# Kernel optimization log

Hardware: AMD Instinct MI355X
Metric: run time of the kernel (lower is better)

Reference implementation:

```python
import math
import jax, jax.numpy as jnp
import numpy as np

HEAD_SIZE = 64
DEPTH = 0

def lambda_init_fn(depth):
    depth = depth + 1
    return 0.8 - 0.6 * math.exp(-0.3 * depth)

def setup_inputs() -> dict:
    key = jax.random.key(0)
    ks = jax.random.split(key, 9)
    B, T, C = 4, 4096, 1024
    H2 = 2 * HEAD_SIZE  # 128
    return {
        "x":  jax.random.normal(ks[0], (B, T, C), dtype=jnp.float32),
        "Wq": jax.random.normal(ks[1], (C, H2), dtype=jnp.float32) * (C ** -0.5),
        "Wk": jax.random.normal(ks[2], (C, H2), dtype=jnp.float32) * (C ** -0.5),
        "Wv": jax.random.normal(ks[3], (C, H2), dtype=jnp.float32) * (C ** -0.5),
        "lambda_q1": jax.random.normal(ks[4], (HEAD_SIZE,), dtype=jnp.float32) * 0.1,
        "lambda_q2": jax.random.normal(ks[5], (HEAD_SIZE,), dtype=jnp.float32) * 0.1,
        "lambda_k1": jax.random.normal(ks[6], (HEAD_SIZE,), dtype=jnp.float32) * 0.1,
        "lambda_k2": jax.random.normal(ks[7], (HEAD_SIZE,), dtype=jnp.float32) * 0.1,
    }

def reference(x, Wq, Wk, Wv, lambda_q1, lambda_q2, lambda_k1, lambda_k2):
    B, T, C = x.shape
    q = x @ Wq  # (B,T,2*hs)
    k = x @ Wk
    v = x @ Wv  # (B,T,2*hs)
    q1, q2 = jnp.split(q, 2, axis=-1)
    k1, k2 = jnp.split(k, 2, axis=-1)
    scale = 1.0 / math.sqrt(HEAD_SIZE)
    w1 = jnp.einsum('btd,bsd->bts', q1, k1) * scale  # (B,T,T)
    w2 = jnp.einsum('btd,bsd->bts', q2, k2) * scale
    causal = jnp.tril(jnp.ones((T, T), dtype=bool))
    neg_inf = jnp.float32(-jnp.inf)
    w1 = jnp.where(causal, w1, neg_inf)
    w2 = jnp.where(causal, w2, neg_inf)
    lam1 = jnp.exp(jnp.sum(lambda_q1 * lambda_k1))
    lam2 = jnp.exp(jnp.sum(lambda_q2 * lambda_k2))
    lam = lam1 - lam2 + lambda_init_fn(DEPTH)
    weights = jax.nn.softmax(w1, axis=-1) - lam * jax.nn.softmax(w2, axis=-1)
    out = jnp.einsum('bts,bsd->btd', weights, v)  # (B,T,2*hs)
    return out
```

## Files before the change

### kernel.cpp

```cpp
#include <hip/hip_runtime.h>
#include <hip/hip_bf16.h>

typedef __bf16 bf16x8 __attribute__((ext_vector_type(8)));
typedef float f32x4 __attribute__((ext_vector_type(4)));

#define LAMBDA_INIT 0.3555090675909693f
#define CEXP 0.18033688011112042f

#define K_OFF   ((size_t)16384 * 128)
#define VT_OFF  ((size_t)2 * 16384 * 128)
#define PART_OFF_BYTES ((size_t)12582912)
#define REC_FLOATS 4160

__device__ __forceinline__ unsigned short f2bf(float f) {
    __hip_bfloat16 h = __float2bfloat16(f);
    unsigned short u;
    __builtin_memcpy(&u, &h, 2);
    return u;
}
__device__ __forceinline__ float bf2f(unsigned short u) {
    unsigned int x = ((unsigned int)u) << 16;
    float f;
    __builtin_memcpy(&f, &x, 4);
    return f;
}
__device__ __forceinline__ unsigned int cvt_pk_bf16(float a, float b) {
    unsigned int r;
    asm volatile("v_cvt_pk_bf16_f32 %0, %1, %2" : "=v"(r) : "v"(a), "v"(b));
    return r;
}

__global__ __launch_bounds__(256) void prep_wt(
    const float* __restrict__ Wq, const float* __restrict__ Wk,
    const float* __restrict__ Wv, unsigned short* __restrict__ WT) {
    const int kt = blockIdx.x, nt = blockIdx.y, mat = blockIdx.z;
    const float* W = (mat == 0) ? Wq : (mat == 1) ? Wk : Wv;
    unsigned short* O = WT + (size_t)mat * 128 * 1024;
    __shared__ float tb[64][65];
    const int r = threadIdx.x >> 2, c4 = (threadIdx.x & 3) * 16;
    for (int j = 0; j < 4; ++j) {
        float4 v = *(const float4*)&W[(size_t)(kt * 64 + r) * 128 + nt * 64 + c4 + j * 4];
        tb[r][c4 + j * 4 + 0] = v.x;
        tb[r][c4 + j * 4 + 1] = v.y;
        tb[r][c4 + j * 4 + 2] = v.z;
        tb[r][c4 + j * 4 + 3] = v.w;
    }
    __syncthreads();
    unsigned short tmp[16];
    for (int j = 0; j < 16; ++j) tmp[j] = f2bf(tb[c4 + j][r]);
    *(uint4*)&O[(size_t)(nt * 64 + r) * 1024 + kt * 64 + c4] = *(uint4*)&tmp[0];
    *(uint4*)&O[(size_t)(nt * 64 + r) * 1024 + kt * 64 + c4 + 8] = *(uint4*)&tmp[8];
}

__global__ __launch_bounds__(256) void qkv_gemm(
    const float* __restrict__ x, const unsigned short* __restrict__ WT,
    unsigned short* __restrict__ qkv) {
    const int tid = threadIdx.x;
    const int l = tid & 63, w = tid >> 6;
    const int g = l >> 4, i16 = l & 15;
    const int row0 = blockIdx.x * 64;
    const int mat = blockIdx.y;
    const unsigned short* Wt = WT + (size_t)mat * 128 * 1024;

    __shared__ unsigned short xs[64][72];
    __shared__ unsigned short wt[128][72];

    f32x4 acc[8];
    const f32x4 z4 = {0.f, 0.f, 0.f, 0.f};
    for (int nb = 0; nb < 8; ++nb) acc[nb] = z4;

    const int xr = tid >> 4;
    const int xc = (tid & 15) * 4;
    const int wn = tid >> 3;
    const int wk8 = (tid & 7) * 8;
    const float* xp0 = &x[(size_t)(row0 + xr) * 1024 + xc];
    const unsigned short* wp0 = &Wt[(size_t)wn * 1024 + wk8];

    float4 fx0, fx1, fx2, fx3;
    uint4 fw0, fw1, fw2, fw3;

#define QKV_ISSUE(k0_) do {                                                 \
        fx0 = *(const float4*)&xp0[(k0_)];                                  \
        fx1 = *(const float4*)&xp0[16 * 1024 + (k0_)];                      \
        fx2 = *(const float4*)&xp0[32 * 1024 + (k0_)];                      \
        fx3 = *(const float4*)&xp0[48 * 1024 + (k0_)];                      \
        fw0 = *(const uint4*)&wp0[(k0_)];                                   \
        fw1 = *(const uint4*)&wp0[32 * 1024 + (k0_)];                       \
        fw2 = *(const uint4*)&wp0[64 * 1024 + (k0_)];                       \
        fw3 = *(const uint4*)&wp0[96 * 1024 + (k0_)];                       \
    } while (0)

#define QKV_STORE() do {                                                    \
        *(ushort4*)&xs[xr +  0][xc] = make_ushort4(f2bf(fx0.x), f2bf(fx0.y), f2bf(fx0.z), f2bf(fx0.w)); \
        *(ushort4*)&xs[xr + 16][xc] = make_ushort4(f2bf(fx1.x), f2bf(fx1.y), f2bf(fx1.z), f2bf(fx1.w)); \
        *(ushort4*)&xs[xr + 32][xc] = make_ushort4(f2bf(fx2.x), f2bf(fx2.y), f2bf(fx2.z), f2bf(fx2.w)); \
        *(ushort4*)&xs[xr + 48][xc] = make_ushort4(f2bf(fx3.x), f2bf(fx3.y), f2bf(fx3.z), f2bf(fx3.w)); \
        *(uint4*)&wt[wn +  0][wk8] = fw0;                                   \
        *(uint4*)&wt[wn + 32][wk8] = fw1;                                   \
        *(uint4*)&wt[wn + 64][wk8] = fw2;                                   \
        *(uint4*)&wt[wn + 96][wk8] = fw3;                                   \
    } while (0)

    QKV_ISSUE(0);
    #pragma unroll 1
    for (int k0 = 0; k0 < 1024; k0 += 64) {
        __syncthreads();
        QKV_STORE();
        if (k0 + 64 < 1024) QKV_ISSUE(k0 + 64);
        __syncthreads();

        bf16x8 af0 = *(const bf16x8*)&xs[w * 16 + i16][8 * g];
        bf16x8 af1 = *(const bf16x8*)&xs[w * 16 + i16][32 + 8 * g];
        #pragma unroll
        for (int nb = 0; nb < 8; ++nb) {
            bf16x8 b0 = *(const bf16x8*)&wt[nb * 16 + i16][8 * g];
            bf16x8 b1 = *(const bf16x8*)&wt[nb * 16 + i16][32 + 8 * g];
            acc[nb] = __builtin_amdgcn_mfma_f32_16x16x32_bf16(af0, b0, acc[nb], 0, 0, 0);
            acc[nb] = __builtin_amdgcn_mfma_f32_16x16x32_bf16(af1, b1, acc[nb], 0, 0, 0);
        }
    }
#undef QKV_ISSUE
#undef QKV_STORE

    __syncthreads();
    unsigned short(*ts)[136] = (unsigned short(*)[136]) & wt[0][0];
    const float qscale = (mat == 0) ? CEXP : 1.0f;
    for (int nb = 0; nb < 8; ++nb)
        for (int r = 0; r < 4; ++r)
            ts[w * 16 + g * 4 + r][nb * 16 + i16] = f2bf(acc[nb][r] * qscale);
    __syncthreads();

    const int bq = row0 >> 12;
    const int s = (row0 >> 6) & 63;
    if (mat == 0) {
        unsigned short* outp = qkv + (size_t)row0 * 128;
        #pragma unroll
        for (int it = 0; it < 4; ++it) {
            int tr = it * 16 + (tid >> 4), dv0 = (tid & 15) * 8;
            *(uint4*)&outp[tr * 128 + dv0] = *(const uint4*)&ts[tr][dv0];
        }
    } else if (mat == 1) {
        unsigned short* kimg = qkv + K_OFF + ((size_t)(bq * 64 + s) * 2) * 4096;
        #pragma unroll
        for (int it = 0; it < 4; ++it) {
            int lin = it * 256 + tid;
            int branch_ = (lin >> 9) & 1;
            int region = (lin >> 6) & 7;
            int slot = lin & 63;
            int row = (region >> 1) * 16 + (slot & 15);
            int d = branch_ * 64 + (region & 1) * 32 + (slot >> 4) * 8;
            uint4 vv = *(const uint4*)&ts[row][d];
            *(uint4*)&kimg[(size_t)branch_ * 4096 + (region * 64 + slot) * 8] = vv;
        }
    } else {
        unsigned short* vimg = qkv + VT_OFF + (size_t)(bq * 64 + s) * 8192;
        #pragma unroll
        for (int it = 0; it < 4; ++it) {
            int lin = it * 256 + tid;
            int region = lin >> 6;
            int slot = lin & 63;
            int dv = (region >> 1) * 16 + (slot & 15);
            int kv0 = (region & 1) * 32 + (slot >> 4) * 8;
            unsigned short tmp[8];
            #pragma unroll
            for (int e = 0; e < 8; ++e) tmp[e] = ts[kv0 + e][dv];
            *(uint4*)&vimg[(region * 64 + slot) * 8] = *(uint4*)tmp;
        }
    }
}

__global__ __launch_bounds__(256, 3) void diff_attn_pair(
    const unsigned short* __restrict__ q, const unsigned short* __restrict__ kimg,
    const unsigned short* __restrict__ vimg,
    float* __restrict__ part, int ncs) {
    const int bx = blockIdx.x, b = blockIdx.y;
    const int c = blockIdx.z >> 1, branch = blockIdx.z & 1;
    const int bxe = (c & 1) ? (31 - bx) : bx;
    const int t_o = 63 - 2 * bxe, t_e = t_o - 1;
    const int n = t_o + 1;
    const int s_lo = (c * n) >> ncs, smax = ((c + 1) * n) >> ncs;

    if (s_lo >= smax) return;

    const int tid = threadIdx.x;
    const int l = tid & 63, w = tid >> 6;
    const int gq = l >> 4, i16 = l & 15;
    const float NEGINF = -__builtin_inff();

    __shared__ unsigned short ksf[4096];
    __shared__ unsigned short psf[8192];

    float* recA = part + ((((size_t)(b * 64 + t_e) << ncs) + c) * 2 + branch) * REC_FLOATS;
    float* recB = part + ((((size_t)(b * 64 + t_o) << ncs) + c) * 2 + branch) * REC_FLOATS;
    const bool emptyA = (s_lo > t_e);

    const size_t bbase = (size_t)b * 4096;
    const unsigned short* kimg_b = kimg + (size_t)b * 524288;
    const unsigned short* vimg_b = vimg + (size_t)b * 524288;
    const int tid8 = tid * 8;
    const int l8 = l * 8;
    const f32x4 z4 = {0.f, 0.f, 0.f, 0.f};

    bf16x8 qfA[2], qfB[2];
    #pragma unroll
    for (int cc = 0; cc < 2; ++cc) {
        qfA[cc] = *(const bf16x8*)&q[(bbase + t_e * 64 + w * 16 + i16) * 128 + branch * 64 + cc * 32 + 8 * gq];
        qfB[cc] = *(const bf16x8*)&q[(bbase + t_o * 64 + w * 16 + i16) * 128 + branch * 64 + cc * 32 + 8 * gq];
    }

    float lsumA = 0.f, lsumB = 0.f;
    f32x4 acc[2][4][2];
    for (int qs = 0; qs < 2; ++qs)
        for (int qg = 0; qg < 4; ++qg)
            for (int j = 0; j < 2; ++j) acc[qs][qg][j] = z4;

    int pdst[4];
    #pragma unroll
    for (int cb = 0; cb < 4; ++cb)
        pdst[cb] = ((w * 2 + (cb >> 1)) * 64 + ((cb & 1) * 2 + (gq >> 1)) * 16 + i16) * 8 + (gq & 1) * 4;

    uint4 kr0, kr1;
    bf16x8 vb00, vb01, vb10, vb11;

#define K_ISSUE(s_) do {                                                            \
        const unsigned short* kp = &kimg_b[((size_t)(s_) * 2 + branch) * 4096];     \
        kr0 = *(const uint4*)&kp[tid8];                                             \
        kr1 = *(const uint4*)&kp[tid8 + 2048];                                      \
    } while (0)
#define V_ISSUE(s_) do {                                                            \
        const unsigned short* vp = &vimg_b[(size_t)(s_) * 8192 + w * 2048];         \
        vb00 = *(const bf16x8*)&vp[l8];                                             \
        vb01 = *(const bf16x8*)&vp[512 + l8];                                       \
        vb10 = *(const bf16x8*)&vp[1024 + l8];                                      \
        vb11 = *(const bf16x8*)&vp[1536 + l8];                                      \
    } while (0)

    K_ISSUE(s_lo);
    V_ISSUE(s_lo);
    #pragma unroll 1
    for (int s = s_lo; s < smax; ++s) {
        __syncthreads();
        *(uint4*)&ksf[tid8] = kr0;
        *(uint4*)&ksf[tid8 + 2048] = kr1;
        if (s + 1 < smax) K_ISSUE(s + 1);
        __syncthreads();
        const bool aAct = (s != t_o);

        if (aAct) {
            f32x4 sc[4];
            for (int cb = 0; cb < 4; ++cb) sc[cb] = z4;
            __builtin_amdgcn_s_setprio(1);
            #pragma unroll
            for (int cb = 0; cb < 4; ++cb)
                for (int cc = 0; cc < 2; ++cc) {
                    bf16x8 kf = *(const bf16x8*)&ksf[((cb * 2 + cc) * 64 + l) * 8];
                    sc[cb] = __builtin_amdgcn_mfma_f32_16x16x32_bf16(kf, qfA[cc], sc[cb], 0, 0, 0);
                }
            __builtin_amdgcn_s_setprio(0);
            if (s == t_e) {
                int ql = w * 16 + i16;
                for (int cb = 0; cb < 4; ++cb)
                    for (int r = 0; r < 4; ++r)
                        if (cb * 16 + gq * 4 + r > ql) sc[cb][r] = NEGINF;
            }
            #pragma unroll
            for (int cb = 0; cb < 4; ++cb) {
                float p0 = exp2f(sc[cb][0]);
                float p1 = exp2f(sc[cb][1]);
                float p2 = exp2f(sc[cb][2]);
                float p3 = exp2f(sc[cb][3]);
                lsumA += (p0 + p1) + (p2 + p3);
                uint2 pw;
                pw.x = cvt_pk_bf16(p0, p1);
                pw.y = cvt_pk_bf16(p2, p3);
                *(uint2*)&psf[pdst[cb]] = pw;
            }
        }
        {
            f32x4 sc[4];
            for (int cb = 0; cb < 4; ++cb) sc[cb] = z4;
            __builtin_amdgcn_s_setprio(1);
            #pragma unroll
            for (int cb = 0; cb < 4; ++cb)
                for (int cc = 0; cc < 2; ++cc) {
                    bf16x8 kf = *(const bf16x8*)&ksf[((cb * 2 + cc) * 64 + l) * 8];
                    sc[cb] = __builtin_amdgcn_mfma_f32_16x16x32_bf16(kf, qfB[cc], sc[cb], 0, 0, 0);
                }
            __builtin_amdgcn_s_setprio(0);
            if (s == t_o) {
                int ql = w * 16 + i16;
                for (int cb = 0; cb < 4; ++cb)
                    for (int r = 0; r < 4; ++r)
                        if (cb * 16 + gq * 4 + r > ql) sc[cb][r] = NEGINF;
            }
            #pragma unroll
            for (int cb = 0; cb < 4; ++cb) {
                float p0 = exp2f(sc[cb][0]);
                float p1 = exp2f(sc[cb][1]);
                float p2 = exp2f(sc[cb][2]);
                float p3 = exp2f(sc[cb][3]);
                lsumB += (p0 + p1) + (p2 + p3);
                uint2 pw;
                pw.x = cvt_pk_bf16(p0, p1);
                pw.y = cvt_pk_bf16(p2, p3);
                *(uint2*)&psf[4096 + pdst[cb]] = pw;
            }
        }
        __syncthreads();

        __builtin_amdgcn_s_setprio(1);
        if (aAct) {
            #pragma unroll
            for (int qg = 0; qg < 4; ++qg) {
                bf16x8 pa0 = *(const bf16x8*)&psf[(qg * 2 + 0) * 512 + l8];
                bf16x8 pa1 = *(const bf16x8*)&psf[(qg * 2 + 1) * 512 + l8];
                acc[0][qg][0] = __builtin_amdgcn_mfma_f32_16x16x32_bf16(pa0, vb00, acc[0][qg][0], 0, 0, 0);
                acc[0][qg][0] = __builtin_amdgcn_mfma_f32_16x16x32_bf16(pa1, vb01, acc[0][qg][0], 0, 0, 0);
                acc[0][qg][1] = __builtin_amdgcn_mfma_f32_16x16x32_bf16(pa0, vb10, acc[0][qg][1], 0, 0, 0);
                acc[0][qg][1] = __builtin_amdgcn_mfma_f32_16x16x32_bf16(pa1, vb11, acc[0][qg][1], 0, 0, 0);
            }
        }
        #pragma unroll
        for (int qg = 0; qg < 4; ++qg) {
            bf16x8 pa0 = *(const bf16x8*)&psf[4096 + (qg * 2 + 0) * 512 + l8];
            bf16x8 pa1 = *(const bf16x8*)&psf[4096 + (qg * 2 + 1) * 512 + l8];
            acc[1][qg][0] = __builtin_amdgcn_mfma_f32_16x16x32_bf16(pa0, vb00, acc[1][qg][0], 0, 0, 0);
            acc[1][qg][0] = __builtin_amdgcn_mfma_f32_16x16x32_bf16(pa1, vb01, acc[1][qg][0], 0, 0, 0);
            acc[1][qg][1] = __builtin_amdgcn_mfma_f32_16x16x32_bf16(pa0, vb10, acc[1][qg][1], 0, 0, 0);
            acc[1][qg][1] = __builtin_amdgcn_mfma_f32_16x16x32_bf16(pa1, vb11, acc[1][qg][1], 0, 0, 0);
        }
        __builtin_amdgcn_s_setprio(0);
        if (s + 1 < smax) V_ISSUE(s + 1);
    }
#undef K_ISSUE
#undef V_ISSUE

    lsumA += __shfl_xor(lsumA, 16);
    lsumA += __shfl_xor(lsumA, 32);
    lsumB += __shfl_xor(lsumB, 16);
    lsumB += __shfl_xor(lsumB, 32);
    if (!emptyA) {
        if (gq == 0) recA[w * 16 + i16] = lsumA;
        unsigned short* OA = (unsigned short*)(recA + 64);
        for (int qg = 0; qg < 4; ++qg)
            for (int j = 0; j < 2; ++j)
                for (int r = 0; r < 4; ++r)
                    OA[(qg * 16 + gq * 4 + r) * 128 + (w * 2 + j) * 16 + i16] = f2bf(acc[0][qg][j][r]);
    }
    {
        if (gq == 0) recB[w * 16 + i16] = lsumB;
        unsigned short* OB = (unsigned short*)(recB + 64);
        for (int qg = 0; qg < 4; ++qg)
            for (int j = 0; j < 2; ++j)
                for (int r = 0; r < 4; ++r)
                    OB[(qg * 16 + gq * 4 + r) * 128 + (w * 2 + j) * 16 + i16] = f2bf(acc[1][qg][j][r]);
    }
}

__global__ __launch_bounds__(256) void diff_combine(
    const float* __restrict__ part,
    const float* __restrict__ lq1, const float* __restrict__ lq2,
    const float* __restrict__ lk1, const float* __restrict__ lk2,
    float* __restrict__ out, int ncs) {
    const int t = blockIdx.x, b = blockIdx.y;
    const int tid = threadIdx.x;
    const int nc = 1 << ncs;
    const int n = (t | 1) + 1;
    __shared__ float sl[2][64];
    __shared__ float s_lam;

    const float* recbase = part + (((size_t)(b * 64 + t) << ncs)) * 2 * REC_FLOATS;

    if (tid < 64) {
        float s1 = lq1[tid] * lk1[tid];
        float s2 = lq2[tid] * lk2[tid];
        for (int off = 32; off > 0; off >>= 1) {
            s1 += __shfl_xor(s1, off);
            s2 += __shfl_xor(s2, off);
        }
        if (tid == 0) s_lam = expf(s1) - expf(s2) + LAMBDA_INIT;
    }
    if (tid < 128) {
        int r = tid & 63, br = tid >> 6;
        float acc = 0.f;
        for (int c = 0; c < nc; ++c) {
            int lo = (c * n) >> ncs, hi = ((c + 1) * n) >> ncs;
            if (lo >= hi || lo > t) continue;
            acc += recbase[(c * 2 + br) * REC_FLOATS + r];
        }
        sl[br][r] = acc;
    }
    __syncthreads();
    const float lam = s_lam;

    float* op = out + ((size_t)b * 4096 + (size_t)t * 64) * 128;
    for (int grp = 0; grp < 4; ++grp) {
        int gid = grp * 256 + tid;
        int e = gid * 8;
        int row = e >> 7;
        float o1[8] = {0, 0, 0, 0, 0, 0, 0, 0}, o2[8] = {0, 0, 0, 0, 0, 0, 0, 0};
        for (int c = 0; c < nc; ++c) {
            int lo = (c * n) >> ncs, hi = ((c + 1) * n) >> ncs;
            if (lo >= hi || lo > t) continue;
            const unsigned short* O0 = (const unsigned short*)(recbase + (c * 2 + 0) * REC_FLOATS + 64);
            const unsigned short* O1 = (const unsigned short*)(recbase + (c * 2 + 1) * REC_FLOATS + 64);
            uint4 u0 = *(const uint4*)&O0[e];
            uint4 u1 = *(const uint4*)&O1[e];
            const unsigned short* e0 = (const unsigned short*)&u0;
            const unsigned short* e1 = (const unsigned short*)&u1;
            #pragma unroll
            for (int j = 0; j < 8; ++j) {
                o1[j] += bf2f(e0[j]);
                o2[j] += bf2f(e1[j]);
            }
        }
        float l1inv = 1.0f / sl[0][row], l2inv = 1.0f / sl[1][row];
        float res[8];
        #pragma unroll
        for (int j = 0; j < 8; ++j) res[j] = o1[j] * l1inv - lam * o2[j] * l2inv;
        *(float4*)&op[e] = *(float4*)&res[0];
        *(float4*)&op[e + 4] = *(float4*)&res[4];
    }
}

extern "C" void kernel_launch(void* const* d_in, const int* in_sizes, int n_in,
                              void* d_out, int out_size, void* d_ws, size_t ws_size,
                              hipStream_t stream) {
    const float* x   = (const float*)d_in[0];
    const float* Wq  = (const float*)d_in[1];
    const float* Wk  = (const float*)d_in[2];
    const float* Wv  = (const float*)d_in[3];
    const float* lq1 = (const float*)d_in[4];
    const float* lq2 = (const float*)d_in[5];
    const float* lk1 = (const float*)d_in[6];
    const float* lk2 = (const float*)d_in[7];
    float* out = (float*)d_out;
    unsigned short* qkv = (unsigned short*)d_ws;

    const int ncs = 2;
    const size_t part_bytes = (size_t)256 * (1 << ncs) * 2 * REC_FLOATS * 4;
    float* part = (float*)((char*)d_ws + PART_OFF_BYTES);
    unsigned short* WT = (unsigned short*)((char*)d_ws + PART_OFF_BYTES + part_bytes);

    prep_wt<<<dim3(16, 2, 3), 256, 0, stream>>>(Wq, Wk, Wv, WT);
    qkv_gemm<<<dim3(256, 3), 256, 0, stream>>>(x, WT, qkv);

    const unsigned short* qb = qkv;
    const unsigned short* kb = qkv + K_OFF;
    const unsigned short* vtb = qkv + VT_OFF;
    diff_attn_pair<<<dim3(32, 4, 2 << ncs), 256, 0, stream>>>(qb, kb, vtb, part, ncs);
    diff_combine<<<dim3(64, 4), 256, 0, stream>>>(part, lq1, lq2, lk1, lk2, out, ncs);
}
```

Measured before the change: 96.18 us.

## Double-buffer K tile in attention and deepen QKV GEMM prefetch

The QKV projection GEMM now keeps two k-slabs of global loads in flight, using alternating register sets, and gets a 3-blocks-per-CU launch bound. In the attention kernel the K shared tile is double-buffered, which removes one barrier per step. The QK^T MFMAs for both query tiles are interleaved so they can share each K fragment load. In exchange the kernels use more registers and LDS, which could cut occupancy, and the A-tile QK MFMAs now run even on steps where that tile is inactive.

```diff
diff --git a/kernel.cpp b/kernel.cpp
--- a/kernel.cpp
+++ b/kernel.cpp
@@ -52,7 +52,7 @@
     *(uint4*)&O[(size_t)(nt * 64 + r) * 1024 + kt * 64 + c4 + 8] = *(uint4*)&tmp[8];
 }
 
-__global__ __launch_bounds__(256) void qkv_gemm(
+__global__ __launch_bounds__(256, 3) void qkv_gemm(
     const float* __restrict__ x, const unsigned short* __restrict__ WT,
     unsigned short* __restrict__ qkv) {
     const int tid = threadIdx.x;
@@ -76,51 +76,61 @@
     const float* xp0 = &x[(size_t)(row0 + xr) * 1024 + xc];
     const unsigned short* wp0 = &Wt[(size_t)wn * 1024 + wk8];
 
-    float4 fx0, fx1, fx2, fx3;
-    uint4 fw0, fw1, fw2, fw3;
-
-#define QKV_ISSUE(k0_) do {                                                 \
-        fx0 = *(const float4*)&xp0[(k0_)];                                  \
-        fx1 = *(const float4*)&xp0[16 * 1024 + (k0_)];                      \
-        fx2 = *(const float4*)&xp0[32 * 1024 + (k0_)];                      \
-        fx3 = *(const float4*)&xp0[48 * 1024 + (k0_)];                      \
-        fw0 = *(const uint4*)&wp0[(k0_)];                                   \
-        fw1 = *(const uint4*)&wp0[32 * 1024 + (k0_)];                       \
-        fw2 = *(const uint4*)&wp0[64 * 1024 + (k0_)];                       \
-        fw3 = *(const uint4*)&wp0[96 * 1024 + (k0_)];                       \
+    float4 ax0, ax1, ax2, ax3, bx0, bx1, bx2, bx3;
+    uint4 aw0, aw1, aw2, aw3, bw0, bw1, bw2, bw3;
+
+#define QI(k0_, X0, X1, X2, X3, W0, W1, W2, W3) do {                        \
+        X0 = *(const float4*)&xp0[(k0_)];                                   \
+        X1 = *(const float4*)&xp0[16 * 1024 + (k0_)];                       \
+        X2 = *(const float4*)&xp0[32 * 1024 + (k0_)];                       \
+        X3 = *(const float4*)&xp0[48 * 1024 + (k0_)];                       \
+        W0 = *(const uint4*)&wp0[(k0_)];                                    \
+        W1 = *(const uint4*)&wp0[32 * 1024 + (k0_)];                        \
+        W2 = *(const uint4*)&wp0[64 * 1024 + (k0_)];                        \
+        W3 = *(const uint4*)&wp0[96 * 1024 + (k0_)];                        \
     } while (0)
 
-#define QKV_STORE() do {                                                    \
-        *(ushort4*)&xs[xr +  0][xc] = make_ushort4(f2bf(fx0.x), f2bf(fx0.y), f2bf(fx0.z), f2bf(fx0.w)); \
-        *(ushort4*)&xs[xr + 16][xc] = make_ushort4(f2bf(fx1.x), f2bf(fx1.y), f2bf(fx1.z), f2bf(fx1.w)); \
-        *(ushort4*)&xs[xr + 32][xc] = make_ushort4(f2bf(fx2.x), f2bf(fx2.y), f2bf(fx2.z), f2bf(fx2.w)); \
-        *(ushort4*)&xs[xr + 48][xc] = make_ushort4(f2bf(fx3.x), f2bf(fx3.y), f2bf(fx3.z), f2bf(fx3.w)); \
-        *(uint4*)&wt[wn +  0][wk8] = fw0;                                   \
-        *(uint4*)&wt[wn + 32][wk8] = fw1;                                   \
-        *(uint4*)&wt[wn + 64][wk8] = fw2;                                   \
-        *(uint4*)&wt[wn + 96][wk8] = fw3;                                   \
+#define QS(X0, X1, X2, X3, W0, W1, W2, W3) do {                             \
+        *(ushort4*)&xs[xr +  0][xc] = make_ushort4(f2bf(X0.x), f2bf(X0.y), f2bf(X0.z), f2bf(X0.w)); \
+        *(ushort4*)&xs[xr + 16][xc] = make_ushort4(f2bf(X1.x), f2bf(X1.y), f2bf(X1.z), f2bf(X1.w)); \
+        *(ushort4*)&xs[xr + 32][xc] = make_ushort4(f2bf(X2.x), f2bf(X2.y), f2bf(X2.z), f2bf(X2.w)); \
+        *(ushort4*)&xs[xr + 48][xc] = make_ushort4(f2bf(X3.x), f2bf(X3.y), f2bf(X3.z), f2bf(X3.w)); \
+        *(uint4*)&wt[wn +  0][wk8] = W0;                                    \
+        *(uint4*)&wt[wn + 32][wk8] = W1;                                    \
+        *(uint4*)&wt[wn + 64][wk8] = W2;                                    \
+        *(uint4*)&wt[wn + 96][wk8] = W3;                                    \
     } while (0)
 
-    QKV_ISSUE(0);
+#define QMFMA() do {                                                        \
+        bf16x8 af0 = *(const bf16x8*)&xs[w * 16 + i16][8 * g];              \
+        bf16x8 af1 = *(const bf16x8*)&xs[w * 16 + i16][32 + 8 * g];         \
+        _Pragma("unroll")                                                   \
+        for (int nb = 0; nb < 8; ++nb) {                                    \
+            bf16x8 b0 = *(const bf16x8*)&wt[nb * 16 + i16][8 * g];          \
+            bf16x8 b1 = *(const bf16x8*)&wt[nb * 16 + i16][32 + 8 * g];     \
+            acc[nb] = __builtin_amdgcn_mfma_f32_16x16x32_bf16(af0, b0, acc[nb], 0, 0, 0); \
+            acc[nb] = __builtin_amdgcn_mfma_f32_16x16x32_bf16(af1, b1, acc[nb], 0, 0, 0); \
+        }                                                                   \
+    } while (0)
+
+    QI(0, ax0, ax1, ax2, ax3, aw0, aw1, aw2, aw3);
+    QI(64, bx0, bx1, bx2, bx3, bw0, bw1, bw2, bw3);
     #pragma unroll 1
-    for (int k0 = 0; k0 < 1024; k0 += 64) {
-        __syncthreads();
-        QKV_STORE();
-        if (k0 + 64 < 1024) QKV_ISSUE(k0 + 64);
-        __syncthreads();
-
-        bf16x8 af0 = *(const bf16x8*)&xs[w * 16 + i16][8 * g];
-        bf16x8 af1 = *(const bf16x8*)&xs[w * 16 + i16][32 + 8 * g];
-        #pragma unroll
-        for (int nb = 0; nb < 8; ++nb) {
-            bf16x8 b0 = *(const bf16x8*)&wt[nb * 16 + i16][8 * g];
-            bf16x8 b1 = *(const bf16x8*)&wt[nb * 16 + i16][32 + 8 * g];
-            acc[nb] = __builtin_amdgcn_mfma_f32_16x16x32_bf16(af0, b0, acc[nb], 0, 0, 0);
-            acc[nb] = __builtin_amdgcn_mfma_f32_16x16x32_bf16(af1, b1, acc[nb], 0, 0, 0);
-        }
-    }
-#undef QKV_ISSUE
-#undef QKV_STORE
+    for (int k0 = 0; k0 < 1024; k0 += 128) {
+        __syncthreads();
+        QS(ax0, ax1, ax2, ax3, aw0, aw1, aw2, aw3);
+        if (k0 + 128 < 1024) QI(k0 + 128, ax0, ax1, ax2, ax3, aw0, aw1, aw2, aw3);
+        __syncthreads();
+        QMFMA();
+        __syncthreads();
+        QS(bx0, bx1, bx2, bx3, bw0, bw1, bw2, bw3);
+        if (k0 + 192 < 1024) QI(k0 + 192, bx0, bx1, bx2, bx3, bw0, bw1, bw2, bw3);
+        __syncthreads();
+        QMFMA();
+    }
+#undef QI
+#undef QS
+#undef QMFMA
 
     __syncthreads();
     unsigned short(*ts)[136] = (unsigned short(*)[136]) & wt[0][0];
@@ -187,7 +197,7 @@
     const int gq = l >> 4, i16 = l & 15;
     const float NEGINF = -__builtin_inff();
 
-    __shared__ unsigned short ksf[4096];
+    __shared__ unsigned short ksf[2][4096];
     __shared__ unsigned short psf[8192];
 
     float* recA = part + ((((size_t)(b * 64 + t_e) << ncs) + c) * 2 + branch) * REC_FLOATS;
@@ -237,38 +247,40 @@
 
     K_ISSUE(s_lo);
     V_ISSUE(s_lo);
+    int pb = 0;
     #pragma unroll 1
     for (int s = s_lo; s < smax; ++s) {
-        __syncthreads();
-        *(uint4*)&ksf[tid8] = kr0;
-        *(uint4*)&ksf[tid8 + 2048] = kr1;
+        *(uint4*)&ksf[pb][tid8] = kr0;
+        *(uint4*)&ksf[pb][tid8 + 2048] = kr1;
         if (s + 1 < smax) K_ISSUE(s + 1);
         __syncthreads();
         const bool aAct = (s != t_o);
 
+        f32x4 scA[4], scB[4];
+        for (int cb = 0; cb < 4; ++cb) { scA[cb] = z4; scB[cb] = z4; }
+        __builtin_amdgcn_s_setprio(1);
+        #pragma unroll
+        for (int cb = 0; cb < 4; ++cb)
+            for (int cc = 0; cc < 2; ++cc) {
+                bf16x8 kf = *(const bf16x8*)&ksf[pb][((cb * 2 + cc) * 64 + l) * 8];
+                scA[cb] = __builtin_amdgcn_mfma_f32_16x16x32_bf16(kf, qfA[cc], scA[cb], 0, 0, 0);
+                scB[cb] = __builtin_amdgcn_mfma_f32_16x16x32_bf16(kf, qfB[cc], scB[cb], 0, 0, 0);
+            }
+        __builtin_amdgcn_s_setprio(0);
+
         if (aAct) {
-            f32x4 sc[4];
-            for (int cb = 0; cb < 4; ++cb) sc[cb] = z4;
-            __builtin_amdgcn_s_setprio(1);
-            #pragma unroll
-            for (int cb = 0; cb < 4; ++cb)
-                for (int cc = 0; cc < 2; ++cc) {
-                    bf16x8 kf = *(const bf16x8*)&ksf[((cb * 2 + cc) * 64 + l) * 8];
-                    sc[cb] = __builtin_amdgcn_mfma_f32_16x16x32_bf16(kf, qfA[cc], sc[cb], 0, 0, 0);
-                }
-            __builtin_amdgcn_s_setprio(0);
             if (s == t_e) {
                 int ql = w * 16 + i16;
                 for (int cb = 0; cb < 4; ++cb)
                     for (int r = 0; r < 4; ++r)
-                        if (cb * 16 + gq * 4 + r > ql) sc[cb][r] = NEGINF;
+                        if (cb * 16 + gq * 4 + r > ql) scA[cb][r] = NEGINF;
             }
             #pragma unroll
             for (int cb = 0; cb < 4; ++cb) {
-                float p0 = exp2f(sc[cb][0]);
-                float p1 = exp2f(sc[cb][1]);
-                float p2 = exp2f(sc[cb][2]);
-                float p3 = exp2f(sc[cb][3]);
+                float p0 = exp2f(scA[cb][0]);
+                float p1 = exp2f(scA[cb][1]);
+                float p2 = exp2f(scA[cb][2]);
+                float p3 = exp2f(scA[cb][3]);
                 lsumA += (p0 + p1) + (p2 + p3);
                 uint2 pw;
                 pw.x = cvt_pk_bf16(p0, p1);
@@ -277,28 +289,18 @@
             }
         }
         {
-            f32x4 sc[4];
-            for (int cb = 0; cb < 4; ++cb) sc[cb] = z4;
-            __builtin_amdgcn_s_setprio(1);
-            #pragma unroll
-            for (int cb = 0; cb < 4; ++cb)
-                for (int cc = 0; cc < 2; ++cc) {
-                    bf16x8 kf = *(const bf16x8*)&ksf[((cb * 2 + cc) * 64 + l) * 8];
-                    sc[cb] = __builtin_amdgcn_mfma_f32_16x16x32_bf16(kf, qfB[cc], sc[cb], 0, 0, 0);
-                }
-            __builtin_amdgcn_s_setprio(0);
             if (s == t_o) {
                 int ql = w * 16 + i16;
                 for (int cb = 0; cb < 4; ++cb)
                     for (int r = 0; r < 4; ++r)
-                        if (cb * 16 + gq * 4 + r > ql) sc[cb][r] = NEGINF;
+                        if (cb * 16 + gq * 4 + r > ql) scB[cb][r] = NEGINF;
             }
             #pragma unroll
             for (int cb = 0; cb < 4; ++cb) {
-                float p0 = exp2f(sc[cb][0]);
-                float p1 = exp2f(sc[cb][1]);
-                float p2 = exp2f(sc[cb][2]);
-                float p3 = exp2f(sc[cb][3]);
+                float p0 = exp2f(scB[cb][0]);
+                float p1 = exp2f(scB[cb][1]);
+                float p2 = exp2f(scB[cb][2]);
+                float p3 = exp2f(scB[cb][3]);
                 lsumB += (p0 + p1) + (p2 + p3);
                 uint2 pw;
                 pw.x = cvt_pk_bf16(p0, p1);
@@ -331,6 +333,7 @@
         }
         __builtin_amdgcn_s_setprio(0);
         if (s + 1 < smax) V_ISSUE(s + 1);
+        pb ^= 1;
     }
 #undef K_ISSUE
 #undef V_ISSUE
```

Result: no change. 97.82 us (+1.7%).
